# Performance work log

Hardware: AMD Instinct MI355X
Metric: run time of the kernel (lower is better)

Reference implementation:

```python
import jax, jax.numpy as jnp
import numpy as np

N_QUBITS = 21
N_LAYERS = 3

# standard CNOT (control = first wire), reshaped for tensor contraction
_CNOT = np.array([[1, 0, 0, 0],
                  [0, 1, 0, 0],
                  [0, 0, 0, 1],
                  [0, 0, 1, 0]], dtype=np.complex64).reshape(2, 2, 2, 2)


def _rot(phi, theta, omega):
    """Rot(phi, theta, omega) = RZ(omega) RY(theta) RZ(phi), 2x2 complex64."""
    c = jnp.cos(theta * 0.5)
    s = jnp.sin(theta * 0.5)
    ep = jnp.exp(-0.5j * (phi + omega))   # e^{-i(phi+omega)/2}
    em = jnp.exp(0.5j * (phi - omega))    # e^{+i(phi-omega)/2}
    row0 = jnp.stack([ep * c, -em * s])
    row1 = jnp.stack([jnp.conj(em) * s, jnp.conj(ep) * c])
    return jnp.stack([row0, row1])


def _apply_1q(U, state, q):
    # contract gate with qubit axis q of state (shape (2,)*n)
    return jnp.moveaxis(jnp.tensordot(U, state, axes=((1,), (q,))), 0, q)


def _apply_cnot(state, q):
    # CNOT on adjacent qubits (q, q+1)
    out = jnp.tensordot(jnp.asarray(_CNOT), state, axes=((2, 3), (q, q + 1)))
    return jnp.moveaxis(out, (0, 1), (q, q + 1))


def _classifier(param, feat):
    n_layers, n_qubits = param.shape[0], param.shape[1]
    state = feat.astype(jnp.complex64).reshape((2,) * n_qubits)
    for i in range(n_layers):
        # layer of single-qubit Rot gates (== kron of per-qubit 2x2 unitaries)
        for j in range(n_qubits):
            U = _rot(param[i, j, 0], param[i, j, 1], param[i, j, 2])
            state = _apply_1q(U, state, j)
        # CNOT_layer: first pairs (0,1),(2,3),... then pairs (1,2),(3,4),...
        for q in range(0, n_qubits - 1, 2):
            state = _apply_cnot(state, q)
        for q in range(1, n_qubits - 1, 2):
            state = _apply_cnot(state, q)
    # sum over even flat indices == last qubit in |0>
    amp0 = state[..., 0]
    return jnp.sum(amp0.real ** 2 + amp0.imag ** 2)


def setup_inputs() -> dict:
    key = jax.random.key(0)
    k1, k2 = jax.random.split(key)
    feat = jax.random.normal(k1, (2 ** N_QUBITS,), dtype=jnp.float32)
    param = jax.random.uniform(k2, (N_LAYERS, N_QUBITS, 3),
                               dtype=jnp.float32,
                               minval=0.0, maxval=2.0 * np.pi)
    return {"feat": feat, "param": param}


def reference(feat, param):
    return _classifier(param, feat)
```

## Files before the change

kernel.cpp:

```cpp
#include <hip/hip_runtime.h>
#include <hip/hip_fp16.h>


typedef __attribute__((ext_vector_type(2))) float f2;

union H4 { int4 i4; __half2 h[4]; };
union H2 { int2 i2; __half2 h[2]; };

__device__ __forceinline__ f2 mkf2(float a, float b) { f2 r; r.x = a; r.y = b; return r; }

__device__ __forceinline__ unsigned SWZ(unsigned i) {
    return i ^ ((i >> 4) & 0xFu) ^ ((i >> 8) & 0xFu);
}
__device__ __forceinline__ unsigned f1(unsigned x, unsigned m) {
    return x ^ ((x >> 1) & m);
}
__device__ __forceinline__ unsigned f2fold(unsigned x, unsigned mA, unsigned mB) {
    unsigned t = x ^ ((x >> 1) & mA);
    return t ^ ((t >> 1) & mB);
}

__device__ __forceinline__ void crot(const f2 u00, const f2 u01,
                                     const f2 u10, const f2 u11,
                                     f2& a, f2& b) {
    const f2 sa = mkf2(-a.y, a.x);
    const f2 sb = mkf2(-b.y, b.x);
    f2 na = u00.x * a;
    na += u00.y * sa;
    na += u01.x * b;
    na += u01.y * sb;
    f2 nb = u10.x * a;
    nb += u10.y * sa;
    nb += u11.x * b;
    nb += u11.y * sb;
    a = na; b = nb;
}

__device__ __forceinline__ void apply4(f2 v[16], const f2* gU,
                                       int id0, int id1, int id2, int id3) {
    const int ids[4] = {id0, id1, id2, id3};
#pragma unroll
    for (int kk = 0; kk < 4; ++kk) {
        const int id = ids[kk];
        if (id < 0) continue;
        const f2 u00 = gU[4*id+0], u01 = gU[4*id+1];
        const f2 u10 = gU[4*id+2], u11 = gU[4*id+3];
#pragma unroll
        for (int x = 0; x < 16; ++x)
            if (!(x & (1 << kk)))
                crot(u00, u01, u10, u11, v[x], v[x | (1 << kk)]);
    }
}

__device__ __forceinline__ void prep_gates_lds(const float* __restrict__ param,
                                               f2* gU, unsigned tid) {
    if (tid < 63) {
        float phi = param[3*tid+0], th = param[3*tid+1], om = param[3*tid+2];
        float s, c;   __sincosf(0.5f*th, &s, &c);
        float sp, cp; __sincosf(-0.5f*(phi+om), &sp, &cp);
        float sm, cm; __sincosf( 0.5f*(phi-om), &sm, &cm);
        gU[4*tid+0] = mkf2( cp*c,  sp*c);
        gU[4*tid+1] = mkf2(-cm*s, -sm*s);
        gU[4*tid+2] = mkf2( cm*s, -sm*s);
        gU[4*tid+3] = mkf2( cp*c, -sp*c);
    }
}

__device__ __forceinline__ unsigned E1A (unsigned t, unsigned r){ return (t<<4)|r; }
__device__ __forceinline__ unsigned E2A (unsigned t, unsigned r){ return ((t>>4)<<8)|(r<<4)|(t&15u); }
__device__ __forceinline__ unsigned E3A (unsigned t, unsigned r){ return ((t>>8)<<12)|(r<<8)|(t&255u); }
__device__ __forceinline__ unsigned E4A (unsigned t, unsigned r){
    return (t&127u) | (((t>>7)&3u)<<10) | ((r&1u)<<7) | (((r>>1)&1u)<<8) | (((r>>2)&1u)<<9) | (((r>>3)&1u)<<12);
}
__device__ __forceinline__ unsigned E5A (unsigned t, unsigned r){
    return (t&31u) | (((t>>5)&7u)<<7) | (((t>>8)&1u)<<12) | ((r&1u)<<5) | (((r>>1)&1u)<<6) | (((r>>2)&1u)<<10) | (((r>>3)&1u)<<11);
}
__device__ __forceinline__ unsigned E6A (unsigned t, unsigned r){ return (t&1u) | (((t>>1)&255u)<<5) | (r<<1); }
__device__ __forceinline__ unsigned E7A (unsigned t, unsigned r){
    return ((t&63u)<<1) | (((t>>6)&7u)<<10) | (r&1u) | (((r>>1)&1u)<<7) | (((r>>2)&1u)<<8) | (((r>>3)&1u)<<9);
}
__device__ __forceinline__ unsigned E8A (unsigned t, unsigned r){ return (t&7u) | (((t>>3)&63u)<<7) | ((r&15u)<<3); }
__device__ __forceinline__ unsigned E11A(unsigned t, unsigned r){
    return (r&7u) | (((r>>3)&1u)<<8) | ((t&15u)<<9) | ((t>>4)<<3);
}
__device__ __forceinline__ unsigned E1Bn(unsigned t, unsigned r){ return (t&127u) | (r<<7); }
__device__ __forceinline__ unsigned E2Bn(unsigned t, unsigned r){ return (t&7u) | (r<<3) | ((t>>3)<<7); }
__device__ __forceinline__ unsigned E5Bn(unsigned t, unsigned r){
    return (t&3u) | ((r&1u)<<2) | (((t>>2)&31u)<<3) | (((r>>1)&1u)<<8) | (((r>>2)&1u)<<9) | (((r>>3)&1u)<<10);
}
__device__ __forceinline__ unsigned E6Bn(unsigned t, unsigned r){ return (t&15u) | (r<<4) | ((t>>4)<<8); }
__device__ __forceinline__ unsigned E7Bn(unsigned t, unsigned r){ return (r&15u) | (t<<4); }

#define PHASE(BUF, EW, ER) do { \
    _Pragma("unroll") for (int r = 0; r < 16; ++r) { unsigned e_ = (EW); BUF[SWZ(e_)] = v[r]; } \
    __syncthreads(); \
    _Pragma("unroll") for (int r = 0; r < 16; ++r) { unsigned e_ = (ER); v[r] = BUF[SWZ(e_)]; } \
    } while (0)

__global__ __launch_bounds__(512, 2) void sweepA(const float* __restrict__ feat,
                                                 const float* __restrict__ param,
                                                 __half2* __restrict__ zbuf,
                                                 float* __restrict__ out) {
    __shared__ f2 sh0[8192];
    __shared__ f2 sh1[8192];
    __shared__ f2 gU[252];
    const unsigned tid = threadIdx.x;
    const unsigned F = blockIdx.x;
    if (F == 0 && tid == 0) out[0] = 0.0f;

    float4 fraw[4];
    {
        const float4* fp = (const float4*)(feat + (((size_t)F) << 13) + (tid << 4));
#pragma unroll
        for (int c = 0; c < 4; ++c) fraw[c] = fp[c];
    }
    prep_gates_lds(param, gU, tid);

    f2 v[16];
#pragma unroll
    for (int c = 0; c < 4; ++c) {
        v[4*c+0] = mkf2(fraw[c].x, 0.f); v[4*c+1] = mkf2(fraw[c].y, 0.f);
        v[4*c+2] = mkf2(fraw[c].z, 0.f); v[4*c+3] = mkf2(fraw[c].w, 0.f);
    }
    __syncthreads();
    apply4(v, gU, 20, 19, 18, 17);
    PHASE(sh0, E1A(tid,r), E2A(tid,r));
    apply4(v, gU, 16, 15, 14, 13);
    PHASE(sh1, E2A(tid,r), E3A(tid,r));
    apply4(v, gU, 12, 11, 10, 9);
    PHASE(sh0, E3A(tid,r), f2fold(E4A(tid,r), 0x155u, 0x2AAu));
    apply4(v, gU, 34, 33, 32, 8);
    PHASE(sh1, E4A(tid,r), f2fold(E5A(tid,r), 0x400u, 0x800u));
    apply4(v, gU, 36, 35, 31, 30);
    PHASE(sh0, E5A(tid,r), f2fold(E6A(tid,r), 0x140u, 0x2A0u));
    apply4(v, gU, 40, 39, 38, 37);
    PHASE(sh1, E6A(tid,r), f2fold(E7A(tid,r), 0x014u, 0x00Au));
    apply4(v, gU, 41, 55, 54, 53);
    PHASE(sh0, E7A(tid,r), f1(E8A(tid,r), 0x081u));
    apply4(v, gU, 59, 58, 57, 56);
    PHASE(sh1, E8A(tid,r), f2fold(E11A(tid,r), 0x050u, 0x028u));
    apply4(v, gU, 62, 61, 60, -1);

    {
        int2* zb2 = (int2*)zbuf;
        const unsigned sbase = (tid & 15u) | (F << 4) | ((tid >> 4) << 15);
#pragma unroll
        for (unsigned g = 0; g < 8; ++g) {
            H2 y;
            y.h[0] = __float22half2_rn(make_float2(v[g].x,      v[g].y));
            y.h[1] = __float22half2_rn(make_float2(v[g | 8u].x, v[g | 8u].y));
            zb2[sbase | (g << 12)] = y.i2;
        }
    }
}

__global__ __launch_bounds__(128, 2) void sweepB(const __half2* __restrict__ zbuf,
                                                 const float* __restrict__ param,
                                                 float* __restrict__ out) {
    __shared__ f2 sh0[2048];
    __shared__ f2 sh1[2048];
    __shared__ f2 gU[252];
    __shared__ float wsum[2];
    const unsigned tid = threadIdx.x;
    const unsigned b = ((blockIdx.x & 7u) << 6) | (blockIdx.x >> 3);
    const unsigned B8 = (b >> 2) << 1;
    const unsigned t0 = B8 ^ ((B8 >> 1) & 5u);
    const unsigned Bp8 = t0 ^ ((t0 >> 1) & 2u);
    const unsigned zbase = (b & 1u) | (((b >> 1) & 1u) << 1) | (Bp8 << 13);

    __half2 raw[16];
    {
        const __half2* zp = zbuf + zbase;
#pragma unroll
        for (int r = 0; r < 16; ++r) {
            unsigned ee = tid | ((unsigned)r << 7);
            raw[r] = zp[(size_t)ee << 2];
        }
    }
    prep_gates_lds(param, gU, tid);

    f2 v[16];
#pragma unroll
    for (int r = 0; r < 16; ++r) {
        float2 t2 = __half22float2(raw[r]);
        v[r] = mkf2(t2.x, t2.y);
    }
    __syncthreads();
    apply4(v, gU, 3, 2, 1, 0);
    PHASE(sh1, E1Bn(tid,r), f1(E2Bn(tid,r), 0x280u));
    apply4(v, gU, 7, 6, 5, 4);
    PHASE(sh0, E2Bn(tid,r), f2fold(E1Bn(tid,r), 0x154u, 0x028u));
    apply4(v, gU, 24, 23, 22, 21);
    PHASE(sh1, E1Bn(tid,r), f1(E2Bn(tid,r), 0x280u));
    apply4(v, gU, 28, 27, 26, 25);
    PHASE(sh0, E2Bn(tid,r), f2fold(E5Bn(tid,r), 0x150u, 0x028u));
    apply4(v, gU, 29, 44, 43, 42);
    PHASE(sh1, E5Bn(tid,r), f2fold(E6Bn(tid,r), 0x005u, 0x002u));
    apply4(v, gU, 48, 47, 46, 45);
    PHASE(sh0, E6Bn(tid,r), E7Bn(tid,r));
    apply4(v, gU, 52, 51, 50, 49);
    float acc = 0.f;
#pragma unroll
    for (int r = 0; r < 16; ++r) acc += v[r].x*v[r].x + v[r].y*v[r].y;
    for (int off = 32; off; off >>= 1) acc += __shfl_down(acc, off);
    if ((tid & 63u) == 0) wsum[tid >> 6] = acc;
    __syncthreads();
    if (tid == 0) atomicAdd(out, wsum[0] + wsum[1]);
}

extern "C" void kernel_launch(void* const* d_in, const int* in_sizes, int n_in,
                              void* d_out, int out_size, void* d_ws, size_t ws_size,
                              hipStream_t stream) {
    const float* feat  = (const float*)d_in[0];
    const float* param = (const float*)d_in[1];
    float* out = (float*)d_out;
    __half2* zbuf = (__half2*)d_ws;

    sweepA<<<256, 512, 0, stream>>>(feat, param, zbuf, out);
    sweepB<<<512, 128, 0, stream>>>(zbuf, param, out);
}
```

Before: 46.05 us.

## Restructure sweepA to 1024 threads holding 8 amplitudes each with 3-qubit phases

sweepA moves from 512 threads with 16 amplitudes per thread to 1024 threads with 8 amplitudes per thread. Gates are applied three qubits at a time through new LDS index maps and transposes. The aim is more parallelism per block and less register pressure, so more wavefronts can hide latency. The cost is more LDS exchange phases and barriers (11 instead of 8). Launch bounds drop the two-blocks-per-CU hint, and 128KB of shared memory per block already caps residency at one block.

```diff
diff --git a/kernel.cpp b/kernel.cpp
--- a/kernel.cpp
+++ b/kernel.cpp
@@ -36,6 +36,22 @@
     a = na; b = nb;
 }
 
+__device__ __forceinline__ void apply3(f2 v[8], const f2* gU,
+                                       int id0, int id1, int id2) {
+    const int ids[3] = {id0, id1, id2};
+#pragma unroll
+    for (int kk = 0; kk < 3; ++kk) {
+        const int id = ids[kk];
+        if (id < 0) continue;
+        const f2 u00 = gU[4*id+0], u01 = gU[4*id+1];
+        const f2 u10 = gU[4*id+2], u11 = gU[4*id+3];
+#pragma unroll
+        for (int x = 0; x < 8; ++x)
+            if (!(x & (1 << kk)))
+                crot(u00, u01, u10, u11, v[x], v[x | (1 << kk)]);
+    }
+}
+
 __device__ __forceinline__ void apply4(f2 v[16], const f2* gU,
                                        int id0, int id1, int id2, int id3) {
     const int ids[4] = {id0, id1, id2, id3};
@@ -66,22 +82,27 @@
     }
 }
 
-__device__ __forceinline__ unsigned E1A (unsigned t, unsigned r){ return (t<<4)|r; }
-__device__ __forceinline__ unsigned E2A (unsigned t, unsigned r){ return ((t>>4)<<8)|(r<<4)|(t&15u); }
-__device__ __forceinline__ unsigned E3A (unsigned t, unsigned r){ return ((t>>8)<<12)|(r<<8)|(t&255u); }
-__device__ __forceinline__ unsigned E4A (unsigned t, unsigned r){
-    return (t&127u) | (((t>>7)&3u)<<10) | ((r&1u)<<7) | (((r>>1)&1u)<<8) | (((r>>2)&1u)<<9) | (((r>>3)&1u)<<12);
-}
-__device__ __forceinline__ unsigned E5A (unsigned t, unsigned r){
-    return (t&31u) | (((t>>5)&7u)<<7) | (((t>>8)&1u)<<12) | ((r&1u)<<5) | (((r>>1)&1u)<<6) | (((r>>2)&1u)<<10) | (((r>>3)&1u)<<11);
-}
-__device__ __forceinline__ unsigned E6A (unsigned t, unsigned r){ return (t&1u) | (((t>>1)&255u)<<5) | (r<<1); }
-__device__ __forceinline__ unsigned E7A (unsigned t, unsigned r){
-    return ((t&63u)<<1) | (((t>>6)&7u)<<10) | (r&1u) | (((r>>1)&1u)<<7) | (((r>>2)&1u)<<8) | (((r>>3)&1u)<<9);
-}
-__device__ __forceinline__ unsigned E8A (unsigned t, unsigned r){ return (t&7u) | (((t>>3)&63u)<<7) | ((r&15u)<<3); }
-__device__ __forceinline__ unsigned E11A(unsigned t, unsigned r){
-    return (r&7u) | (((r>>3)&1u)<<8) | ((t&15u)<<9) | ((t>>4)<<3);
+__device__ __forceinline__ unsigned M1 (unsigned t, unsigned r){ return (t<<3)|r; }
+__device__ __forceinline__ unsigned M2 (unsigned t, unsigned r){ return (t&7u) | (r<<3) | ((t>>3)<<6); }
+__device__ __forceinline__ unsigned M3 (unsigned t, unsigned r){ return (t&63u) | (r<<6) | ((t>>6)<<9); }
+__device__ __forceinline__ unsigned M4 (unsigned t, unsigned r){ return (t&511u) | (r<<9) | ((t>>9)<<12); }
+__device__ __forceinline__ unsigned M5 (unsigned t, unsigned r){ return (t&127u) | (r<<7) | ((t>>7)<<10); }
+__device__ __forceinline__ unsigned M6 (unsigned t, unsigned r){
+    return (t&31u) | ((r&1u)<<5) | (((r>>1)&1u)<<6) | (((t>>5)&31u)<<7) | (((r>>2)&1u)<<12);
+}
+__device__ __forceinline__ unsigned M7 (unsigned t, unsigned r){
+    return (t&15u) | ((r&1u)<<4) | (((t>>4)&31u)<<5) | (((r>>1)&1u)<<10) | (((r>>2)&1u)<<11) | ((t>>9)<<12);
+}
+__device__ __forceinline__ unsigned M8 (unsigned t, unsigned r){ return (t&1u) | (r<<1) | ((t>>1)<<4); }
+__device__ __forceinline__ unsigned M9 (unsigned t, unsigned r){
+    return (r&1u) | ((t&63u)<<1) | (((r>>1)&1u)<<7) | (((r>>2)&1u)<<8) | ((t>>6)<<9);
+}
+__device__ __forceinline__ unsigned M10(unsigned t, unsigned r){
+    return (t&31u) | ((r&1u)<<5) | (((r>>1)&1u)<<6) | (((t>>5)&3u)<<7) | (((r>>2)&1u)<<9) | ((t>>7)<<10);
+}
+__device__ __forceinline__ unsigned M11(unsigned t, unsigned r){ return (t&3u) | (r<<2) | ((t>>2)<<5); }
+__device__ __forceinline__ unsigned M12(unsigned t, unsigned r){
+    return (r&1u) | (((r>>1)&1u)<<1) | (((t>>4)&63u)<<2) | (((r>>2)&1u)<<8) | ((t&15u)<<9);
 }
 __device__ __forceinline__ unsigned E1Bn(unsigned t, unsigned r){ return (t&127u) | (r<<7); }
 __device__ __forceinline__ unsigned E2Bn(unsigned t, unsigned r){ return (t&7u) | (r<<3) | ((t>>3)<<7); }
@@ -91,16 +112,21 @@
 __device__ __forceinline__ unsigned E6Bn(unsigned t, unsigned r){ return (t&15u) | (r<<4) | ((t>>4)<<8); }
 __device__ __forceinline__ unsigned E7Bn(unsigned t, unsigned r){ return (r&15u) | (t<<4); }
 
-#define PHASE(BUF, EW, ER) do { \
+#define PHASE8(BUF, EW, ER) do { \
+    _Pragma("unroll") for (int r = 0; r < 8; ++r) { unsigned e_ = (EW); BUF[SWZ(e_)] = v[r]; } \
+    __syncthreads(); \
+    _Pragma("unroll") for (int r = 0; r < 8; ++r) { unsigned e_ = (ER); v[r] = BUF[SWZ(e_)]; } \
+    } while (0)
+#define PHASE16(BUF, EW, ER) do { \
     _Pragma("unroll") for (int r = 0; r < 16; ++r) { unsigned e_ = (EW); BUF[SWZ(e_)] = v[r]; } \
     __syncthreads(); \
     _Pragma("unroll") for (int r = 0; r < 16; ++r) { unsigned e_ = (ER); v[r] = BUF[SWZ(e_)]; } \
     } while (0)
 
-__global__ __launch_bounds__(512, 2) void sweepA(const float* __restrict__ feat,
-                                                 const float* __restrict__ param,
-                                                 __half2* __restrict__ zbuf,
-                                                 float* __restrict__ out) {
+__global__ __launch_bounds__(1024) void sweepA(const float* __restrict__ feat,
+                                               const float* __restrict__ param,
+                                               __half2* __restrict__ zbuf,
+                                               float* __restrict__ out) {
     __shared__ f2 sh0[8192];
     __shared__ f2 sh1[8192];
     __shared__ f2 gU[252];
@@ -108,48 +134,53 @@
     const unsigned F = blockIdx.x;
     if (F == 0 && tid == 0) out[0] = 0.0f;
 
-    float4 fraw[4];
+    float4 f0, fA;
     {
-        const float4* fp = (const float4*)(feat + (((size_t)F) << 13) + (tid << 4));
-#pragma unroll
-        for (int c = 0; c < 4; ++c) fraw[c] = fp[c];
+        const float4* fp = (const float4*)(feat + (((size_t)F) << 13) + (tid << 3));
+        f0 = fp[0]; fA = fp[1];
     }
     prep_gates_lds(param, gU, tid);
 
-    f2 v[16];
-#pragma unroll
-    for (int c = 0; c < 4; ++c) {
-        v[4*c+0] = mkf2(fraw[c].x, 0.f); v[4*c+1] = mkf2(fraw[c].y, 0.f);
-        v[4*c+2] = mkf2(fraw[c].z, 0.f); v[4*c+3] = mkf2(fraw[c].w, 0.f);
-    }
+    f2 v[8];
+    v[0] = mkf2(f0.x, 0.f); v[1] = mkf2(f0.y, 0.f);
+    v[2] = mkf2(f0.z, 0.f); v[3] = mkf2(f0.w, 0.f);
+    v[4] = mkf2(fA.x, 0.f); v[5] = mkf2(fA.y, 0.f);
+    v[6] = mkf2(fA.z, 0.f); v[7] = mkf2(fA.w, 0.f);
     __syncthreads();
-    apply4(v, gU, 20, 19, 18, 17);
-    PHASE(sh0, E1A(tid,r), E2A(tid,r));
-    apply4(v, gU, 16, 15, 14, 13);
-    PHASE(sh1, E2A(tid,r), E3A(tid,r));
-    apply4(v, gU, 12, 11, 10, 9);
-    PHASE(sh0, E3A(tid,r), f2fold(E4A(tid,r), 0x155u, 0x2AAu));
-    apply4(v, gU, 34, 33, 32, 8);
-    PHASE(sh1, E4A(tid,r), f2fold(E5A(tid,r), 0x400u, 0x800u));
-    apply4(v, gU, 36, 35, 31, 30);
-    PHASE(sh0, E5A(tid,r), f2fold(E6A(tid,r), 0x140u, 0x2A0u));
-    apply4(v, gU, 40, 39, 38, 37);
-    PHASE(sh1, E6A(tid,r), f2fold(E7A(tid,r), 0x014u, 0x00Au));
-    apply4(v, gU, 41, 55, 54, 53);
-    PHASE(sh0, E7A(tid,r), f1(E8A(tid,r), 0x081u));
-    apply4(v, gU, 59, 58, 57, 56);
-    PHASE(sh1, E8A(tid,r), f2fold(E11A(tid,r), 0x050u, 0x028u));
-    apply4(v, gU, 62, 61, 60, -1);
+
+    apply3(v, gU, 20, 19, 18);
+    PHASE8(sh0, M1(tid,r), M2(tid,r));
+    apply3(v, gU, 17, 16, 15);
+    PHASE8(sh1, M2(tid,r), M3(tid,r));
+    apply3(v, gU, 14, 13, 12);
+    PHASE8(sh0, M3(tid,r), M4(tid,r));
+    apply3(v, gU, 11, 10, 9);
+    PHASE8(sh1, M4(tid,r), f2fold(M5(tid,r), 0x155u, 0x2AAu));
+    apply3(v, gU, 34, 33, 32);
+    PHASE8(sh0, M5(tid,r), M6(tid,r));
+    apply3(v, gU, 36, 35, 8);
+    PHASE8(sh1, M6(tid,r), f2fold(M7(tid,r), 0x400u, 0x800u));
+    apply3(v, gU, 37, 31, 30);
+    PHASE8(sh0, M7(tid,r), f2fold(M8(tid,r), 0x140u, 0x2A0u));
+    apply3(v, gU, 40, 39, 38);
+    PHASE8(sh1, M8(tid,r), f2fold(M9(tid,r), 0x014u, 0x00Au));
+    apply3(v, gU, 41, 55, 54);
+    PHASE8(sh0, M9(tid,r), f1(M10(tid,r), 0x081u));
+    apply3(v, gU, 57, 56, 53);
+    PHASE8(sh1, M10(tid,r), f2fold(M11(tid,r), 0x040u, 0x020u));
+    apply3(v, gU, 60, 59, 58);
+    PHASE8(sh0, M11(tid,r), f2fold(M12(tid,r), 0x010u, 0x008u));
+    apply3(v, gU, 62, 61, -1);
 
     {
         int2* zb2 = (int2*)zbuf;
-        const unsigned sbase = (tid & 15u) | (F << 4) | ((tid >> 4) << 15);
-#pragma unroll
-        for (unsigned g = 0; g < 8; ++g) {
+        const unsigned sbase = (tid & 15u) | (F << 4) | (((tid >> 4) & 63u) << 14);
+#pragma unroll
+        for (unsigned p = 0; p < 4; ++p) {
             H2 y;
-            y.h[0] = __float22half2_rn(make_float2(v[g].x,      v[g].y));
-            y.h[1] = __float22half2_rn(make_float2(v[g | 8u].x, v[g | 8u].y));
-            zb2[sbase | (g << 12)] = y.i2;
+            y.h[0] = __float22half2_rn(make_float2(v[p].x,      v[p].y));
+            y.h[1] = __float22half2_rn(make_float2(v[p | 4u].x, v[p | 4u].y));
+            zb2[sbase | ((p & 1u) << 12) | (((p >> 1) & 1u) << 13)] = y.i2;
         }
     }
 }
@@ -187,17 +218,17 @@
     }
     __syncthreads();
     apply4(v, gU, 3, 2, 1, 0);
-    PHASE(sh1, E1Bn(tid,r), f1(E2Bn(tid,r), 0x280u));
+    PHASE16(sh1, E1Bn(tid,r), f1(E2Bn(tid,r), 0x280u));
     apply4(v, gU, 7, 6, 5, 4);
-    PHASE(sh0, E2Bn(tid,r), f2fold(E1Bn(tid,r), 0x154u, 0x028u));
+    PHASE16(sh0, E2Bn(tid,r), f2fold(E1Bn(tid,r), 0x154u, 0x028u));
     apply4(v, gU, 24, 23, 22, 21);
-    PHASE(sh1, E1Bn(tid,r), f1(E2Bn(tid,r), 0x280u));
+    PHASE16(sh1, E1Bn(tid,r), f1(E2Bn(tid,r), 0x280u));
     apply4(v, gU, 28, 27, 26, 25);
-    PHASE(sh0, E2Bn(tid,r), f2fold(E5Bn(tid,r), 0x150u, 0x028u));
+    PHASE16(sh0, E2Bn(tid,r), f2fold(E5Bn(tid,r), 0x150u, 0x028u));
     apply4(v, gU, 29, 44, 43, 42);
-    PHASE(sh1, E5Bn(tid,r), f2fold(E6Bn(tid,r), 0x005u, 0x002u));
+    PHASE16(sh1, E5Bn(tid,r), f2fold(E6Bn(tid,r), 0x005u, 0x002u));
     apply4(v, gU, 48, 47, 46, 45);
-    PHASE(sh0, E6Bn(tid,r), E7Bn(tid,r));
+    PHASE16(sh0, E6Bn(tid,r), E7Bn(tid,r));
     apply4(v, gU, 52, 51, 50, 49);
     float acc = 0.f;
 #pragma unroll
@@ -216,6 +247,6 @@
     float* out = (float*)d_out;
     __half2* zbuf = (__half2*)d_ws;
 
-    sweepA<<<256, 512, 0, stream>>>(feat, param, zbuf, out);
+    sweepA<<<256, 1024, 0, stream>>>(feat, param, zbuf, out);
     sweepB<<<512, 128, 0, stream>>>(zbuf, param, out);
 }
```

New measurement: 46.27 us. Within noise of the previous version (+0.5%).
